# Kernel tuning notes

Measured on AMD Instinct MI355X. Metric: run time of the kernel, lower is better.

The kernel has to match this reference:

```python
import jax, jax.numpy as jnp
import numpy as np

D_MODEL = 1024
N_HEADS = 16
DIM_HEAD = 64
NUM_MEM_KV = 16
INNER = N_HEADS * DIM_HEAD  # 1024


def setup_inputs() -> dict:
    key = jax.random.key(0)
    ks = jax.random.split(key, 8)
    s = 0.02
    x = jax.random.normal(ks[0], (2, 2048, D_MODEL), dtype=jnp.float32)
    Wq = jax.random.normal(ks[1], (D_MODEL, INNER), dtype=jnp.float32) * s
    Wkv = jax.random.normal(ks[2], (D_MODEL, 2 * INNER), dtype=jnp.float32) * s
    Wo = jax.random.normal(ks[3], (INNER, D_MODEL), dtype=jnp.float32) * s
    pre_proj = jax.random.normal(ks[4], (N_HEADS, N_HEADS), dtype=jnp.float32)
    post_proj = jax.random.normal(ks[5], (N_HEADS, N_HEADS), dtype=jnp.float32)
    mem_k = jax.random.normal(ks[6], (N_HEADS, NUM_MEM_KV, DIM_HEAD), dtype=jnp.float32)
    mem_v = jax.random.normal(ks[7], (N_HEADS, NUM_MEM_KV, DIM_HEAD), dtype=jnp.float32)
    return {"x": x, "Wq": Wq, "Wkv": Wkv, "Wo": Wo,
            "pre_proj": pre_proj, "post_proj": post_proj,
            "mem_k": mem_k, "mem_v": mem_v}


def reference(x, Wq, Wkv, Wo, pre_proj, post_proj, mem_k, mem_v):
    b, n, _ = x.shape
    scale = DIM_HEAD ** -0.5
    # projections (no bias)
    q = x @ Wq                              # [b, n, inner]
    kv = x @ Wkv                            # self-attention: context = x
    k, v = jnp.split(kv, 2, axis=-1)
    split_heads = lambda t: t.reshape(b, n, N_HEADS, DIM_HEAD).transpose(0, 2, 1, 3)
    q, k, v = split_heads(q), split_heads(k), split_heads(v)  # [b, h, n, d]
    # prepend memory key/values along kv axis
    mk = jnp.broadcast_to(mem_k[None], (b, N_HEADS, NUM_MEM_KV, DIM_HEAD))
    mv = jnp.broadcast_to(mem_v[None], (b, N_HEADS, NUM_MEM_KV, DIM_HEAD))
    k = jnp.concatenate([mk, k], axis=2)    # [b, h, j, d], j = mem + n
    v = jnp.concatenate([mv, v], axis=2)
    dots = jnp.einsum('bhid,bhjd->bhij', q, k) * scale
    # pre-softmax talking-heads mixing
    dots = jnp.einsum('bhij,hk->bkij', dots, pre_proj)
    # causal mask with mem-kv offset: triu(ones(i,j), j-i+1)
    i, j = dots.shape[-2], dots.shape[-1]
    causal = jnp.triu(jnp.ones((i, j), dtype=bool), k=j - i + 1)
    mask_value = jnp.finfo(dots.dtype).min
    dots = jnp.where(causal[None, None], mask_value, dots)
    attn = jax.nn.softmax(dots, axis=-1)
    # post-softmax talking-heads mixing
    attn = jnp.einsum('bhij,hk->bkij', attn, post_proj)
    out = jnp.einsum('bhij,bhjd->bhid', attn, v)   # [b, h, n, d]
    out = out.transpose(0, 2, 1, 3).reshape(b, n, INNER)
    return out @ Wo                                # [b, n, d_model]
```

## Files before the change

### kernel.cpp

```cpp
#include <hip/hip_runtime.h>


typedef __attribute__((ext_vector_type(8))) short short8;
typedef __attribute__((ext_vector_type(4))) float floatx4;

#define MFMA16(a, b, c) __builtin_amdgcn_mfma_f32_16x16x32_bf16(a, b, c, 0, 0, 0)
#define BARLDS() __asm__ volatile("s_waitcnt lgkmcnt(0)\n\ts_barrier" ::: "memory")
#define LGKM0() __asm__ volatile("s_waitcnt lgkmcnt(0)" ::: "memory")

static __device__ __forceinline__ unsigned short f2bf(float f) {
  union { float f; unsigned u; } v; v.f = f;
  unsigned r = v.u + 0x7fffu + ((v.u >> 16) & 1u);
  return (unsigned short)(r >> 16);
}
static __device__ __forceinline__ float bf2f(unsigned short h) {
  union { unsigned u; float f; } v; v.u = ((unsigned)h) << 16;
  return v.f;
}

union S8U { short8 v; unsigned short u[8]; };

__global__ __launch_bounds__(256) void conv_bf16(const float* __restrict__ src,
                                                 unsigned short* __restrict__ dst,
                                                 int n8) {
  int tid = blockIdx.x * 256 + threadIdx.x;
  if (tid >= n8) return;
  const float4* s = (const float4*)src + (size_t)tid * 2;
  float4 a = s[0], b = s[1];
  S8U o;
  o.u[0] = f2bf(a.x); o.u[1] = f2bf(a.y); o.u[2] = f2bf(a.z); o.u[3] = f2bf(a.w);
  o.u[4] = f2bf(b.x); o.u[5] = f2bf(b.y); o.u[6] = f2bf(b.z); o.u[7] = f2bf(b.w);
  *(short8*)(dst + (size_t)tid * 8) = o.v;
}

__global__ __launch_bounds__(256) void transW(const float* __restrict__ src, int Ncols,
                                              unsigned short* __restrict__ dst, int dstRowOff) {
  __shared__ float sw[32][33];
  int n0 = blockIdx.x * 32, k0 = blockIdx.y * 32;
  int t = threadIdx.x;
  int lk = t >> 3, n4 = (t & 7) * 4;
  const float* s = src + (size_t)(k0 + lk) * Ncols + n0 + n4;
  sw[lk][n4 + 0] = s[0]; sw[lk][n4 + 1] = s[1];
  sw[lk][n4 + 2] = s[2]; sw[lk][n4 + 3] = s[3];
  __syncthreads();
  int ln = t >> 3, k4 = (t & 7) * 4;
  unsigned o0 = f2bf(sw[k4 + 0][ln]) | ((unsigned)f2bf(sw[k4 + 1][ln]) << 16);
  unsigned o1 = f2bf(sw[k4 + 2][ln]) | ((unsigned)f2bf(sw[k4 + 3][ln]) << 16);
  uint2 pk; pk.x = o0; pk.y = o1;
  *(uint2*)(dst + (size_t)(dstRowOff + n0 + ln) * 1024 + k0 + k4) = pk;
}

__global__ __launch_bounds__(256) void gemm_bt(const unsigned short* __restrict__ A,
                                               const unsigned short* __restrict__ BT,
                                               unsigned short* __restrict__ Cb,
                                               float* __restrict__ Cf,
                                               int M, int N, int K, int f32out) {
  int w = threadIdx.x >> 6, lane = threadIdx.x & 63;
  int quad = lane >> 4, l16 = lane & 15;
  int m0 = blockIdx.x * 128 + (w >> 1) * 64;
  int n0 = blockIdx.y * 128 + (w & 1) * 64;
  floatx4 acc[4][4];
#pragma unroll
  for (int i = 0; i < 4; i++)
#pragma unroll
    for (int j = 0; j < 4; j++) acc[i][j] = (floatx4){0.f, 0.f, 0.f, 0.f};

  for (int kk = 0; kk < K; kk += 32) {
    short8 af[4], bf[4];
#pragma unroll
    for (int t = 0; t < 4; t++) {
      af[t] = *(const short8*)(A + (size_t)(m0 + t * 16 + l16) * K + kk + quad * 8);
      bf[t] = *(const short8*)(BT + (size_t)(n0 + t * 16 + l16) * K + kk + quad * 8);
    }
#pragma unroll
    for (int mt = 0; mt < 4; mt++)
#pragma unroll
      for (int nt = 0; nt < 4; nt++) acc[mt][nt] = MFMA16(af[mt], bf[nt], acc[mt][nt]);
  }
#pragma unroll
  for (int mt = 0; mt < 4; mt++)
#pragma unroll
    for (int nt = 0; nt < 4; nt++)
#pragma unroll
      for (int r = 0; r < 4; r++) {
        size_t row = m0 + mt * 16 + quad * 4 + r;
        size_t col = n0 + nt * 16 + l16;
        if (f32out) Cf[row * N + col] = acc[mt][nt][r];
        else Cb[row * N + col] = f2bf(acc[mt][nt][r]);
      }
}

__global__ __launch_bounds__(256) void fill_K(const unsigned short* __restrict__ qkv,
                                              const float* __restrict__ mem_k,
                                              unsigned short* __restrict__ Kw) {
  int tid = blockIdx.x * 256 + threadIdx.x;
  if (tid >= 2 * 16 * 2064 * 8) return;
  int d0 = (tid & 7) * 8;
  int j = (tid >> 3) % 2064;
  int h = ((tid >> 3) / 2064) & 15;
  int b = (tid >> 3) / (2064 * 16);
  S8U o;
  if (j < 16) {
    const float* s = mem_k + ((size_t)(h * 16 + j) * 64 + d0);
#pragma unroll
    for (int c = 0; c < 8; c++) o.u[c] = f2bf(s[c]);
  } else {
    o.v = *(const short8*)(qkv + (size_t)(b * 2048 + j - 16) * 3072 + 1024 + h * 64 + d0);
  }
  *(short8*)(Kw + ((size_t)(b * 16 + h) * 2064 + j) * 64 + d0) = o.v;
}

__global__ __launch_bounds__(256) void fill_Vt(const unsigned short* __restrict__ qkv,
                                               const float* __restrict__ mem_v,
                                               unsigned short* __restrict__ Vt) {
  __shared__ float sv[16][65];
  int jt = blockIdx.x, h = blockIdx.y, b = blockIdx.z;
  int t = threadIdx.x;
  int j = t >> 4, d0 = (t & 15) * 4;
  int jg = jt * 16 + j;
  float v0, v1, v2, v3;
  if (jg < 16) {
    const float* s = mem_v + ((size_t)(h * 16 + jg) * 64 + d0);
    v0 = s[0]; v1 = s[1]; v2 = s[2]; v3 = s[3];
  } else {
    const unsigned short* s = qkv + (size_t)(b * 2048 + jg - 16) * 3072 + 2048 + h * 64 + d0;
    v0 = bf2f(s[0]); v1 = bf2f(s[1]); v2 = bf2f(s[2]); v3 = bf2f(s[3]);
  }
  sv[j][d0 + 0] = v0; sv[j][d0 + 1] = v1; sv[j][d0 + 2] = v2; sv[j][d0 + 3] = v3;
  __syncthreads();
  int d = t >> 2, j4 = (t & 3) * 4;
  unsigned o0 = f2bf(sv[j4 + 0][d]) | ((unsigned)f2bf(sv[j4 + 1][d]) << 16);
  unsigned o1 = f2bf(sv[j4 + 2][d]) | ((unsigned)f2bf(sv[j4 + 3][d]) << 16);
  uint2 pk; pk.x = o0; pk.y = o1;
  *(uint2*)(Vt + ((size_t)(b * 16 + h) * 64 + d) * 2064 + jt * 16 + j4) = pk;
}

__global__ __launch_bounds__(1024) void attn_stats(const unsigned short* __restrict__ qkv,
                                                   const unsigned short* __restrict__ Kw,
                                                   const float* __restrict__ pre,
                                                   float* __restrict__ l_ws) {
  const int c = blockIdx.x, it = blockIdx.y, b = blockIdx.z;
  const int i0 = it * 64;
  const int jmax = i0 + 80;
  const int jc0 = c * 160;
  if (jc0 >= jmax) return;
  const int jend = min(jmax, jc0 + 160);
  const int niter = (jend - jc0 + 31) >> 5;

  __shared__ unsigned short S_lds[64 * 776];

  const int tid = threadIdx.x, w = tid >> 6, lane = tid & 63;
  const int quad = lane >> 4, l16 = lane & 15;
  const int hoff = (quad < 2) ? quad * 8 : 0;

  short8 qa[4][2];
#pragma unroll
  for (int s = 0; s < 4; s++) {
    const unsigned short* p =
        qkv + (size_t)(b * 2048 + i0 + s * 16 + l16) * 3072 + w * 64 + quad * 8;
    qa[s][0] = *(const short8*)p;
    qa[s][1] = *(const short8*)(p + 32);
  }
  short8 preA;
#pragma unroll
  for (int jj = 0; jj < 8; jj++) {
    int h = quad * 8 + jj;
    preA[jj] = (short)((quad < 2) ? f2bf(pre[h * 16 + l16] * 0.125f) : 0);
  }
  const unsigned short* Kb = Kw + (size_t)(b * 16 + w) * 2064 * 64;

  float l_loc[4][4];
#pragma unroll
  for (int i4 = 0; i4 < 4; i4++)
#pragma unroll
    for (int r = 0; r < 4; r++) l_loc[i4][r] = 0.f;

  short8 kf[2][2];
#pragma unroll
  for (int jt = 0; jt < 2; jt++) {
    int jr = min(jc0 + jt * 16 + l16, 2063);
    const unsigned short* kp = Kb + (size_t)jr * 64 + quad * 8;
    kf[jt][0] = *(const short8*)kp;
    kf[jt][1] = *(const short8*)(kp + 32);
  }

  for (int n = 0; n < niter; n++) {
    const int j0 = jc0 + n * 32;
#pragma unroll
    for (int jt = 0; jt < 2; jt++)
#pragma unroll
      for (int s = 0; s < 4; s++) {
        floatx4 a = (floatx4){0.f, 0.f, 0.f, 0.f};
        a = MFMA16(qa[s][0], kf[jt][0], a);
        a = MFMA16(qa[s][1], kf[jt][1], a);
#pragma unroll
        for (int r = 0; r < 4; r++)
          S_lds[(s * 16 + quad * 4 + r) * 776 + (jt * 16 + l16) * 24 + w] = f2bf(a[r]);
      }
    if (n + 1 < niter) {
      const int j0n = j0 + 32;
#pragma unroll
      for (int jt = 0; jt < 2; jt++) {
        int jr = min(j0n + jt * 16 + l16, 2063);
        const unsigned short* kp = Kb + (size_t)jr * 64 + quad * 8;
        kf[jt][0] = *(const short8*)kp;
        kf[jt][1] = *(const short8*)(kp + 32);
      }
    }
    BARLDS();
#pragma unroll
    for (int u = 0; u < 8; u++) {
      const int iloc = u >> 1, jt = u & 1, ii = w * 4 + iloc;
      const short8 bb = *(const short8*)(S_lds + ii * 776 + (jt * 16 + l16) * 24 + hoff);
      floatx4 sp = (floatx4){0.f, 0.f, 0.f, 0.f};
      sp = MFMA16(preA, bb, sp);
      const int jg = j0 + jt * 16 + l16;
      if (jg <= i0 + ii + 16) {
#pragma unroll
        for (int r = 0; r < 4; r++) l_loc[iloc][r] += __expf(sp[r]);
      }
    }
    BARLDS();
  }
#pragma unroll
  for (int iloc = 0; iloc < 4; iloc++)
#pragma unroll
    for (int r = 0; r < 4; r++) {
      float v = l_loc[iloc][r];
      v += __shfl_xor(v, 1);
      v += __shfl_xor(v, 2);
      v += __shfl_xor(v, 4);
      v += __shfl_xor(v, 8);
      if (l16 == 0)
        atomicAdd(l_ws + ((size_t)(b * 2048 + i0 + w * 4 + iloc) * 16 + quad * 4 + r), v);
    }
}

__global__ __launch_bounds__(1024) void attn_av(const unsigned short* __restrict__ qkv,
                                                const unsigned short* __restrict__ Kw,
                                                const unsigned short* __restrict__ Vt,
                                                const float* __restrict__ pre,
                                                const float* __restrict__ post,
                                                const float* __restrict__ l_ws,
                                                float* __restrict__ O_ws) {
  const int c = blockIdx.x, it = blockIdx.y, b = blockIdx.z;
  const int i0 = it * 32;
  const int jmax = i0 + 48;
  const int jc0 = c * 160;
  if (jc0 >= jmax) return;
  const int jend = min(jmax, jc0 + 160);
  const int niter = (jend - jc0 + 31) >> 5;

  __shared__ unsigned short S_lds[32 * 776];
  __shared__ unsigned short Pp_lds[16 * 1288];

  const int tid = threadIdx.x, w = tid >> 6, lane = tid & 63;
  const int quad = lane >> 4, l16 = lane & 15;
  const int hoff = (quad < 2) ? quad * 8 : 0;

  short8 qa[2][2];
#pragma unroll
  for (int s = 0; s < 2; s++) {
    const unsigned short* p =
        qkv + (size_t)(b * 2048 + i0 + s * 16 + l16) * 3072 + w * 64 + quad * 8;
    qa[s][0] = *(const short8*)p;
    qa[s][1] = *(const short8*)(p + 32);
  }
  short8 preA, postA;
#pragma unroll
  for (int jj = 0; jj < 8; jj++) {
    int h = quad * 8 + jj;
    float pv = 0.f, qv = 0.f;
    if (quad < 2) { pv = pre[h * 16 + l16] * 0.125f; qv = post[h * 16 + l16]; }
    preA[jj] = (short)f2bf(pv);
    postA[jj] = (short)f2bf(qv);
  }
  float rl[2][4];
#pragma unroll
  for (int iloc = 0; iloc < 2; iloc++)
#pragma unroll
    for (int r = 0; r < 4; r++)
      rl[iloc][r] = 1.0f / l_ws[(size_t)(b * 2048 + i0 + w * 2 + iloc) * 16 + quad * 4 + r];

  floatx4 oacc[2][4];
#pragma unroll
  for (int g = 0; g < 2; g++)
#pragma unroll
    for (int d = 0; d < 4; d++) oacc[g][d] = (floatx4){0.f, 0.f, 0.f, 0.f};

  const unsigned short* Kb = Kw + (size_t)(b * 16 + w) * 2064 * 64;
  const unsigned short* Vb = Vt + (size_t)(b * 16 + w) * 64 * 2064;

  short8 kf[2][2];
#pragma unroll
  for (int jt = 0; jt < 2; jt++) {
    int jr = min(jc0 + jt * 16 + l16, 2063);
    const unsigned short* kp = Kb + (size_t)jr * 64 + quad * 8;
    kf[jt][0] = *(const short8*)kp;
    kf[jt][1] = *(const short8*)(kp + 32);
  }

  for (int n = 0; n < niter; n++) {
    const int j0 = jc0 + n * 32;
    short8 vf[4];
    {
      const int jc = min(j0 + quad * 8, 2056);
#pragma unroll
      for (int d = 0; d < 4; d++)
        vf[d] = *(const short8*)(Vb + (size_t)(d * 16 + l16) * 2064 + jc);
    }
#pragma unroll
    for (int jt = 0; jt < 2; jt++)
#pragma unroll
      for (int s = 0; s < 2; s++) {
        floatx4 a = (floatx4){0.f, 0.f, 0.f, 0.f};
        a = MFMA16(qa[s][0], kf[jt][0], a);
        a = MFMA16(qa[s][1], kf[jt][1], a);
#pragma unroll
        for (int r = 0; r < 4; r++)
          S_lds[(s * 16 + quad * 4 + r) * 776 + (jt * 16 + l16) * 24 + w] = f2bf(a[r]);
      }
    if (n + 1 < niter) {
      const int j0n = j0 + 32;
#pragma unroll
      for (int jt = 0; jt < 2; jt++) {
        int jr = min(j0n + jt * 16 + l16, 2063);
        const unsigned short* kp = Kb + (size_t)jr * 64 + quad * 8;
        kf[jt][0] = *(const short8*)kp;
        kf[jt][1] = *(const short8*)(kp + 32);
      }
    }
    BARLDS();
#pragma unroll
    for (int u = 0; u < 4; u++) {
      const int iloc = u >> 1, jt = u & 1, ii = w * 2 + iloc;
      const int sc = ii * 776 + (jt * 16 + l16) * 24;
      const short8 bb = *(const short8*)(S_lds + sc + hoff);
      floatx4 sp = (floatx4){0.f, 0.f, 0.f, 0.f};
      sp = MFMA16(preA, bb, sp);
      const int jg = j0 + jt * 16 + l16;
      const bool keep = jg <= (i0 + ii + 16);
#pragma unroll
      for (int r = 0; r < 4; r++)
        S_lds[sc + quad * 4 + r] = f2bf(keep ? __expf(sp[r]) * rl[iloc][r] : 0.f);
    }
    LGKM0();
#pragma unroll
    for (int u = 0; u < 4; u++) {
      const int iloc = u >> 1, jt = u & 1, ii = w * 2 + iloc;
      const int sc = ii * 776 + (jt * 16 + l16) * 24;
      const short8 pf = *(const short8*)(S_lds + sc + hoff);
      floatx4 pp = (floatx4){0.f, 0.f, 0.f, 0.f};
      pp = MFMA16(postA, pf, pp);
#pragma unroll
      for (int r = 0; r < 4; r++)
        Pp_lds[(quad * 4 + r) * 1288 + ii * 40 + jt * 16 + l16] = f2bf(pp[r]);
    }
    BARLDS();
#pragma unroll
    for (int g = 0; g < 2; g++) {
      const short8 paf = *(const short8*)(Pp_lds + w * 1288 + (g * 16 + l16) * 40 + quad * 8);
#pragma unroll
      for (int d = 0; d < 4; d++) oacc[g][d] = MFMA16(paf, vf[d], oacc[g][d]);
    }
  }
#pragma unroll
  for (int g = 0; g < 2; g++)
#pragma unroll
    for (int d = 0; d < 4; d++)
#pragma unroll
      for (int r = 0; r < 4; r++)
        atomicAdd(O_ws + (size_t)(b * 2048 + i0 + g * 16 + quad * 4 + r) * 1024 +
                      w * 64 + d * 16 + l16,
                  oacc[g][d][r]);
}

extern "C" void kernel_launch(void* const* d_in, const int* in_sizes, int n_in,
                              void* d_out, int out_size, void* d_ws, size_t ws_size,
                              hipStream_t stream) {
  (void)in_sizes; (void)n_in; (void)out_size; (void)ws_size;
  const float* x     = (const float*)d_in[0];
  const float* Wq    = (const float*)d_in[1];
  const float* Wkv   = (const float*)d_in[2];
  const float* Wo    = (const float*)d_in[3];
  const float* pre   = (const float*)d_in[4];
  const float* post  = (const float*)d_in[5];
  const float* mem_k = (const float*)d_in[6];
  const float* mem_v = (const float*)d_in[7];
  float* out = (float*)d_out;
  char* ws = (char*)d_ws;

  unsigned short* xb     = (unsigned short*)(ws);
  unsigned short* WbT    = (unsigned short*)(ws + 8388608);
  float*          O_ws   = (float*)(ws);
  unsigned short* qkv    = (unsigned short*)(ws + 16777216);
  unsigned short* WoT    = (unsigned short*)(ws + 16777216);
  unsigned short* Kw     = (unsigned short*)(ws + 41943040);
  unsigned short* Vt     = (unsigned short*)(ws + 50397184);
  float*          l_ws   = (float*)(ws + 58851328);
  unsigned short* attn_b = (unsigned short*)(ws + 58851328);

  conv_bf16<<<2048, 256, 0, stream>>>(x, xb, 524288);
  transW<<<dim3(32, 32), 256, 0, stream>>>(Wq, 1024, WbT, 0);
  transW<<<dim3(64, 32), 256, 0, stream>>>(Wkv, 2048, WbT, 1024);
  gemm_bt<<<dim3(32, 24), 256, 0, stream>>>(xb, WbT, qkv, nullptr, 4096, 3072, 1024, 0);
  fill_K<<<2064, 256, 0, stream>>>(qkv, mem_k, Kw);
  fill_Vt<<<dim3(129, 16, 2), 256, 0, stream>>>(qkv, mem_v, Vt);
  hipMemsetAsync(O_ws, 0, 16777216, stream);
  hipMemsetAsync(l_ws, 0, 262144, stream);
  attn_stats<<<dim3(13, 32, 2), 1024, 0, stream>>>(qkv, Kw, pre, l_ws);
  attn_av<<<dim3(13, 64, 2), 1024, 0, stream>>>(qkv, Kw, Vt, pre, post, l_ws, O_ws);
  conv_bf16<<<2048, 256, 0, stream>>>(O_ws, attn_b, 524288);
  transW<<<dim3(32, 32), 256, 0, stream>>>(Wo, 1024, WoT, 0);
  gemm_bt<<<dim3(32, 8), 256, 0, stream>>>(attn_b, WoT, nullptr, out, 4096, 1024, 1024, 1);
}
```

Baseline: 487.1 us.

## Stage GEMM tiles through LDS with register prefetch and shrink attn_stats row tile

The bf16 GEMM now loads each 128x32 A and B slab cooperatively into padded shared memory, prefetching the next slab into registers, so waves share loads instead of each re-reading global memory. Separately, attn_stats processes 32 query rows per block instead of 64, halving its shared-memory footprint and doubling the grid, and it skips the trailing barrier on the last iteration. The GEMM gains data reuse at the cost of two barriers per k-step. The smaller stats tile adds occupancy and parallelism but recomputes more overlapping causal key ranges per row block.

```diff
diff --git a/kernel.cpp b/kernel.cpp
--- a/kernel.cpp
+++ b/kernel.cpp
@@ -55,22 +55,46 @@
                                                unsigned short* __restrict__ Cb,
                                                float* __restrict__ Cf,
                                                int M, int N, int K, int f32out) {
-  int w = threadIdx.x >> 6, lane = threadIdx.x & 63;
-  int quad = lane >> 4, l16 = lane & 15;
-  int m0 = blockIdx.x * 128 + (w >> 1) * 64;
-  int n0 = blockIdx.y * 128 + (w & 1) * 64;
+  __shared__ unsigned short Al[128 * 40];
+  __shared__ unsigned short Bl[128 * 40];
+  const int t = threadIdx.x;
+  const int w = t >> 6, lane = t & 63;
+  const int quad = lane >> 4, l16 = lane & 15;
+  const int mb = blockIdx.x * 128, nb = blockIdx.y * 128;
+  const int m0 = (w >> 1) * 64, n0 = (w & 1) * 64;
+  const int srow = t >> 1, scol = (t & 1) * 16;
+  const unsigned short* Ag = A + (size_t)(mb + srow) * K + scol;
+  const unsigned short* Bg = BT + (size_t)(nb + srow) * K + scol;
+  unsigned short* Aw = Al + srow * 40 + scol;
+  unsigned short* Bw = Bl + srow * 40 + scol;
+
   floatx4 acc[4][4];
 #pragma unroll
   for (int i = 0; i < 4; i++)
 #pragma unroll
     for (int j = 0; j < 4; j++) acc[i][j] = (floatx4){0.f, 0.f, 0.f, 0.f};
 
+  short8 a0 = *(const short8*)(Ag);
+  short8 a1 = *(const short8*)(Ag + 8);
+  short8 b0 = *(const short8*)(Bg);
+  short8 b1 = *(const short8*)(Bg + 8);
+
   for (int kk = 0; kk < K; kk += 32) {
+    __syncthreads();
+    *(short8*)(Aw) = a0; *(short8*)(Aw + 8) = a1;
+    *(short8*)(Bw) = b0; *(short8*)(Bw + 8) = b1;
+    __syncthreads();
+    if (kk + 32 < K) {
+      a0 = *(const short8*)(Ag + kk + 32);
+      a1 = *(const short8*)(Ag + kk + 40);
+      b0 = *(const short8*)(Bg + kk + 32);
+      b1 = *(const short8*)(Bg + kk + 40);
+    }
     short8 af[4], bf[4];
 #pragma unroll
-    for (int t = 0; t < 4; t++) {
-      af[t] = *(const short8*)(A + (size_t)(m0 + t * 16 + l16) * K + kk + quad * 8);
-      bf[t] = *(const short8*)(BT + (size_t)(n0 + t * 16 + l16) * K + kk + quad * 8);
+    for (int s = 0; s < 4; s++) {
+      af[s] = *(const short8*)(Al + (m0 + s * 16 + l16) * 40 + quad * 8);
+      bf[s] = *(const short8*)(Bl + (n0 + s * 16 + l16) * 40 + quad * 8);
     }
 #pragma unroll
     for (int mt = 0; mt < 4; mt++)
@@ -83,8 +107,8 @@
     for (int nt = 0; nt < 4; nt++)
 #pragma unroll
       for (int r = 0; r < 4; r++) {
-        size_t row = m0 + mt * 16 + quad * 4 + r;
-        size_t col = n0 + nt * 16 + l16;
+        size_t row = mb + m0 + mt * 16 + quad * 4 + r;
+        size_t col = nb + n0 + nt * 16 + l16;
         if (f32out) Cf[row * N + col] = acc[mt][nt][r];
         else Cb[row * N + col] = f2bf(acc[mt][nt][r]);
       }
@@ -140,22 +164,22 @@
                                                    const float* __restrict__ pre,
                                                    float* __restrict__ l_ws) {
   const int c = blockIdx.x, it = blockIdx.y, b = blockIdx.z;
-  const int i0 = it * 64;
-  const int jmax = i0 + 80;
+  const int i0 = it * 32;
+  const int jmax = i0 + 48;
   const int jc0 = c * 160;
   if (jc0 >= jmax) return;
   const int jend = min(jmax, jc0 + 160);
   const int niter = (jend - jc0 + 31) >> 5;
 
-  __shared__ unsigned short S_lds[64 * 776];
+  __shared__ unsigned short S_lds[32 * 776];
 
   const int tid = threadIdx.x, w = tid >> 6, lane = tid & 63;
   const int quad = lane >> 4, l16 = lane & 15;
   const int hoff = (quad < 2) ? quad * 8 : 0;
 
-  short8 qa[4][2];
-#pragma unroll
-  for (int s = 0; s < 4; s++) {
+  short8 qa[2][2];
+#pragma unroll
+  for (int s = 0; s < 2; s++) {
     const unsigned short* p =
         qkv + (size_t)(b * 2048 + i0 + s * 16 + l16) * 3072 + w * 64 + quad * 8;
     qa[s][0] = *(const short8*)p;
@@ -169,9 +193,9 @@
   }
   const unsigned short* Kb = Kw + (size_t)(b * 16 + w) * 2064 * 64;
 
-  float l_loc[4][4];
-#pragma unroll
-  for (int i4 = 0; i4 < 4; i4++)
+  float l_loc[2][4];
+#pragma unroll
+  for (int i4 = 0; i4 < 2; i4++)
 #pragma unroll
     for (int r = 0; r < 4; r++) l_loc[i4][r] = 0.f;
 
@@ -189,7 +213,7 @@
 #pragma unroll
     for (int jt = 0; jt < 2; jt++)
 #pragma unroll
-      for (int s = 0; s < 4; s++) {
+      for (int s = 0; s < 2; s++) {
         floatx4 a = (floatx4){0.f, 0.f, 0.f, 0.f};
         a = MFMA16(qa[s][0], kf[jt][0], a);
         a = MFMA16(qa[s][1], kf[jt][1], a);
@@ -209,8 +233,8 @@
     }
     BARLDS();
 #pragma unroll
-    for (int u = 0; u < 8; u++) {
-      const int iloc = u >> 1, jt = u & 1, ii = w * 4 + iloc;
+    for (int u = 0; u < 4; u++) {
+      const int iloc = u >> 1, jt = u & 1, ii = w * 2 + iloc;
       const short8 bb = *(const short8*)(S_lds + ii * 776 + (jt * 16 + l16) * 24 + hoff);
       floatx4 sp = (floatx4){0.f, 0.f, 0.f, 0.f};
       sp = MFMA16(preA, bb, sp);
@@ -220,10 +244,10 @@
         for (int r = 0; r < 4; r++) l_loc[iloc][r] += __expf(sp[r]);
       }
     }
-    BARLDS();
-  }
-#pragma unroll
-  for (int iloc = 0; iloc < 4; iloc++)
+    if (n + 1 < niter) BARLDS();
+  }
+#pragma unroll
+  for (int iloc = 0; iloc < 2; iloc++)
 #pragma unroll
     for (int r = 0; r < 4; r++) {
       float v = l_loc[iloc][r];
@@ -232,7 +256,7 @@
       v += __shfl_xor(v, 4);
       v += __shfl_xor(v, 8);
       if (l16 == 0)
-        atomicAdd(l_ws + ((size_t)(b * 2048 + i0 + w * 4 + iloc) * 16 + quad * 4 + r), v);
+        atomicAdd(l_ws + ((size_t)(b * 2048 + i0 + w * 2 + iloc) * 16 + quad * 4 + r), v);
     }
 }
 
@@ -408,7 +432,7 @@
   fill_Vt<<<dim3(129, 16, 2), 256, 0, stream>>>(qkv, mem_v, Vt);
   hipMemsetAsync(O_ws, 0, 16777216, stream);
   hipMemsetAsync(l_ws, 0, 262144, stream);
-  attn_stats<<<dim3(13, 32, 2), 1024, 0, stream>>>(qkv, Kw, pre, l_ws);
+  attn_stats<<<dim3(13, 64, 2), 1024, 0, stream>>>(qkv, Kw, pre, l_ws);
   attn_av<<<dim3(13, 64, 2), 1024, 0, stream>>>(qkv, Kw, Vt, pre, post, l_ws, O_ws);
   conv_bf16<<<2048, 256, 0, stream>>>(O_ws, attn_b, 524288);
   transW<<<dim3(32, 32), 256, 0, stream>>>(Wo, 1024, WoT, 0);
```

Result: faster. 420.0 us (-13.8%).
